# Optimization experiments

Hardware: AMD Instinct MI355X
Metric: run time of the kernel (lower is better)

## Reference

```python
import jax, jax.numpy as jnp
import numpy as np

B, L, D, H = 4, 1024, 1024, 16
DH = D // H  # 64
TOPK = 32


def setup_inputs() -> dict:
    key = jax.random.key(0)
    ks = jax.random.split(key, 9)
    s = 1.0 / np.sqrt(D)
    return {
        "x": jax.random.normal(ks[0], (B, L, D), jnp.float32),
        "Wq": jax.random.normal(ks[1], (D, D), jnp.float32) * s,
        "bq": jax.random.normal(ks[2], (D,), jnp.float32) * 0.01,
        "Wk": jax.random.normal(ks[3], (D, D), jnp.float32) * s,
        "bk": jax.random.normal(ks[4], (D,), jnp.float32) * 0.01,
        "Wv": jax.random.normal(ks[5], (D, D), jnp.float32) * s,
        "bv": jax.random.normal(ks[6], (D,), jnp.float32) * 0.01,
        "Wo": jax.random.normal(ks[7], (D, D), jnp.float32) * s,
        "bo": jax.random.normal(ks[8], (D,), jnp.float32) * 0.01,
        "top_k": TOPK,
    }


def reference(x, Wq, bq, Wk, bk, Wv, bv, Wo, bo, top_k):
    b, l, _ = x.shape
    q = (x @ Wq + bq).reshape(b, l, H, DH)
    k = (x @ Wk + bk).reshape(b, l, H, DH)
    v = (x @ Wv + bv).reshape(b, l, H, DH)
    # scores: [B, i, j, h]
    scores = jnp.einsum('bihd,bjhd->bijh', q, k) / np.sqrt(DH).astype(np.float32)
    # softmax over axis 2 (j), as in the original (dim=2 of bijh)
    weights = jax.nn.softmax(scores, axis=2)
    if top_k is not None:
        # top-k along j: move j to last axis -> [B, i, h, j]
        w_t = jnp.swapaxes(weights, 2, 3)
        _, idx = jax.lax.top_k(w_t, top_k)
        mask = jnp.put_along_axis(jnp.zeros_like(w_t), idx, 1.0, axis=-1, inplace=False)
        w_t = w_t * mask
        w_t = w_t / (jnp.sum(w_t, axis=-1, keepdims=True) + 1e-8)
        weights = jnp.swapaxes(w_t, 2, 3)
    attn = jnp.einsum('bijh,bjhd->bihd', weights, v).reshape(b, l, D)
    return attn @ Wo + bo
```

## Files before the change

### kernel.cpp

```cpp
#include <hip/hip_runtime.h>
#include <math.h>

#define B_ 4
#define L_ 1024
#define D_ 1024
#define H_ 16
#define DH_ 64
#define M_ (B_*L_)

typedef _Float16 half8 __attribute__((ext_vector_type(8)));
typedef _Float16 half4 __attribute__((ext_vector_type(4)));
typedef float f32x4 __attribute__((ext_vector_type(4)));

#define MFMA16(a,b,c) __builtin_amdgcn_mfma_f32_16x16x32_f16(a, b, c, 0, 0, 0)

__global__ __launch_bounds__(256) void split_x(const float* __restrict__ x,
                                               _Float16* __restrict__ xh,
                                               _Float16* __restrict__ xl) {
  const int i = blockIdx.x * 256 + threadIdx.x;
  float4 v = ((const float4*)x)[i];
  const float a0 = v.x * 16.f, a1 = v.y * 16.f, a2 = v.z * 16.f, a3 = v.w * 16.f;
  const _Float16 h0 = (_Float16)a0, h1 = (_Float16)a1, h2 = (_Float16)a2, h3 = (_Float16)a3;
  half4 hv, lv;
  hv[0] = h0; hv[1] = h1; hv[2] = h2; hv[3] = h3;
  lv[0] = (_Float16)(a0 - (float)h0);
  lv[1] = (_Float16)(a1 - (float)h1);
  lv[2] = (_Float16)(a2 - (float)h2);
  lv[3] = (_Float16)(a3 - (float)h3);
  ((half4*)xh)[i] = hv;
  ((half4*)xl)[i] = lv;
}

__global__ __launch_bounds__(256) void split_wt(const float* __restrict__ W,
                                                _Float16* __restrict__ Wh,
                                                _Float16* __restrict__ Wl) {
  __shared__ float tile[64][65];
  const int t = threadIdx.x;
  const int tk = blockIdx.x & 15;
  const int tn = blockIdx.x >> 4;
  const int kr = t >> 2, ns = (t & 3) * 16;
  const float* src = W + (size_t)(tk * 64 + kr) * D_ + tn * 64 + ns;
  float4 v0 = ((const float4*)src)[0];
  float4 v1 = ((const float4*)src)[1];
  float4 v2 = ((const float4*)src)[2];
  float4 v3 = ((const float4*)src)[3];
  tile[ns + 0][kr] = v0.x;  tile[ns + 1][kr] = v0.y;  tile[ns + 2][kr] = v0.z;  tile[ns + 3][kr] = v0.w;
  tile[ns + 4][kr] = v1.x;  tile[ns + 5][kr] = v1.y;  tile[ns + 6][kr] = v1.z;  tile[ns + 7][kr] = v1.w;
  tile[ns + 8][kr] = v2.x;  tile[ns + 9][kr] = v2.y;  tile[ns + 10][kr] = v2.z; tile[ns + 11][kr] = v2.w;
  tile[ns + 12][kr] = v3.x; tile[ns + 13][kr] = v3.y; tile[ns + 14][kr] = v3.z; tile[ns + 15][kr] = v3.w;
  __syncthreads();
  const int nr = t >> 2, ks = (t & 3) * 16;
  const float* tr = &tile[nr][ks];
  half8 hv0, hv1, lv0, lv1;
#pragma unroll
  for (int i = 0; i < 8; i++) {
    const float s0 = tr[i] * 512.f;
    const float s1 = tr[i + 8] * 512.f;
    const _Float16 h0 = (_Float16)s0, h1 = (_Float16)s1;
    hv0[i] = h0; hv1[i] = h1;
    lv0[i] = (_Float16)(s0 - (float)h0);
    lv1[i] = (_Float16)(s1 - (float)h1);
  }
  _Float16* dh = Wh + (size_t)(tn * 64 + nr) * D_ + tk * 64 + ks;
  _Float16* dl = Wl + (size_t)(tn * 64 + nr) * D_ + tk * 64 + ks;
  *(half8*)dh = hv0; *(half8*)(dh + 8) = hv1;
  *(half8*)dl = lv0; *(half8*)(dl + 8) = lv1;
}

__device__ __forceinline__ void gemm_f16x3_body(
    const _Float16* __restrict__ Ah, const _Float16* __restrict__ Al,
    const _Float16* __restrict__ Bh, const _Float16* __restrict__ Bl,
    const float* __restrict__ bias, float* __restrict__ Cf,
    _Float16* __restrict__ Ch, _Float16* __restrict__ Cl, const bool f16out) {
  __shared__ __align__(16) _Float16 sA[2][2][128][32];
  __shared__ __align__(16) _Float16 sB[2][2][128][32];
  const int t = threadIdx.x;
  const int lane = t & 63;
  const int wid = t >> 6;
  const int bm = blockIdx.y * 128;
  const int bn = blockIdx.x * 128;

  const int m0 = t >> 2, sp0 = t & 3;
  const int sl0 = sp0 ^ ((m0 >> 1) & 3);
  const int m1 = m0 + 64;
  const _Float16* gA0h = Ah + (size_t)(bm + m0) * D_ + sl0 * 8;
  const _Float16* gA1h = Ah + (size_t)(bm + m1) * D_ + sl0 * 8;
  const _Float16* gA0l = Al + (size_t)(bm + m0) * D_ + sl0 * 8;
  const _Float16* gA1l = Al + (size_t)(bm + m1) * D_ + sl0 * 8;
  const _Float16* gB0h = Bh + (size_t)(bn + m0) * D_ + sl0 * 8;
  const _Float16* gB1h = Bh + (size_t)(bn + m1) * D_ + sl0 * 8;
  const _Float16* gB0l = Bl + (size_t)(bn + m0) * D_ + sl0 * 8;
  const _Float16* gB1l = Bl + (size_t)(bn + m1) * D_ + sl0 * 8;

  half8 rA0h = *(const half8*)(gA0h);
  half8 rA1h = *(const half8*)(gA1h);
  half8 rA0l = *(const half8*)(gA0l);
  half8 rA1l = *(const half8*)(gA1l);
  half8 rB0h = *(const half8*)(gB0h);
  half8 rB1h = *(const half8*)(gB1h);
  half8 rB0l = *(const half8*)(gB0l);
  half8 rB1l = *(const half8*)(gB1l);
  *(half8*)&sA[0][0][m0][sp0 * 8] = rA0h;
  *(half8*)&sA[0][0][m1][sp0 * 8] = rA1h;
  *(half8*)&sA[0][1][m0][sp0 * 8] = rA0l;
  *(half8*)&sA[0][1][m1][sp0 * 8] = rA1l;
  *(half8*)&sB[0][0][m0][sp0 * 8] = rB0h;
  *(half8*)&sB[0][0][m1][sp0 * 8] = rB1h;
  *(half8*)&sB[0][1][m0][sp0 * 8] = rB0l;
  *(half8*)&sB[0][1][m1][sp0 * 8] = rB1l;
  __syncthreads();

  f32x4 acc[4][4];
#pragma unroll
  for (int i = 0; i < 4; i++)
#pragma unroll
    for (int j = 0; j < 4; j++) acc[i][j] = {0.f, 0.f, 0.f, 0.f};

  const int wr = wid >> 1, wc = wid & 1;
  const int l15 = lane & 15;
  const int soff = ((lane >> 4) ^ ((l15 >> 1) & 3)) * 8;

  int p = 0;
  for (int k0 = 0; k0 < 1024; k0 += 32) {
    const bool more = (k0 + 32) < 1024;
    if (more) {
      const int kk = k0 + 32;
      rA0h = *(const half8*)(gA0h + kk);
      rA1h = *(const half8*)(gA1h + kk);
      rA0l = *(const half8*)(gA0l + kk);
      rA1l = *(const half8*)(gA1l + kk);
      rB0h = *(const half8*)(gB0h + kk);
      rB1h = *(const half8*)(gB1h + kk);
      rB0l = *(const half8*)(gB0l + kk);
      rB1l = *(const half8*)(gB1l + kk);
    }
    half8 bh[4], bl[4];
#pragma unroll
    for (int ni = 0; ni < 4; ni++) {
      const int rb = wc * 64 + ni * 16 + l15;
      bh[ni] = *(const half8*)&sB[p][0][rb][soff];
      bl[ni] = *(const half8*)&sB[p][1][rb][soff];
    }
#pragma unroll
    for (int mi = 0; mi < 4; mi++) {
      const int ra = wr * 64 + mi * 16 + l15;
      const half8 ah = *(const half8*)&sA[p][0][ra][soff];
      const half8 al = *(const half8*)&sA[p][1][ra][soff];
#pragma unroll
      for (int ni = 0; ni < 4; ni++) {
        acc[mi][ni] = MFMA16(ah, bh[ni], acc[mi][ni]);
        acc[mi][ni] = MFMA16(ah, bl[ni], acc[mi][ni]);
        acc[mi][ni] = MFMA16(al, bh[ni], acc[mi][ni]);
      }
    }
    if (more) {
      const int q = p ^ 1;
      *(half8*)&sA[q][0][m0][sp0 * 8] = rA0h;
      *(half8*)&sA[q][0][m1][sp0 * 8] = rA1h;
      *(half8*)&sA[q][1][m0][sp0 * 8] = rA0l;
      *(half8*)&sA[q][1][m1][sp0 * 8] = rA1l;
      *(half8*)&sB[q][0][m0][sp0 * 8] = rB0h;
      *(half8*)&sB[q][0][m1][sp0 * 8] = rB1h;
      *(half8*)&sB[q][1][m0][sp0 * 8] = rB0l;
      *(half8*)&sB[q][1][m1][sp0 * 8] = rB1l;
      __syncthreads();
      p = q;
    }
  }

  const float inv = 1.0f / 8192.0f;
  const int orow = bm + wr * 64 + (lane >> 4) * 4;
  const int ocol = bn + wc * 64 + l15;
#pragma unroll
  for (int ni = 0; ni < 4; ni++) {
    const int col = ocol + ni * 16;
    const float bv = bias[col];
#pragma unroll
    for (int mi = 0; mi < 4; mi++) {
      const f32x4 a = acc[mi][ni];
#pragma unroll
      for (int r = 0; r < 4; r++) {
        const size_t idx = (size_t)(orow + mi * 16 + r) * D_ + col;
        const float val = a[r] * inv + bv;
        if (f16out) {
          const float vs = val * 16.0f;
          const _Float16 hh = (_Float16)vs;
          Ch[idx] = hh;
          Cl[idx] = (_Float16)(vs - (float)hh);
        } else {
          Cf[idx] = val;
        }
      }
    }
  }
}

__global__ __launch_bounds__(256, 2) void gemm_qkv_f16(
    const _Float16* __restrict__ xh, const _Float16* __restrict__ xl,
    const _Float16* __restrict__ Whq, const _Float16* __restrict__ Wlq,
    const _Float16* __restrict__ Whk, const _Float16* __restrict__ Wlk,
    const _Float16* __restrict__ Whv, const _Float16* __restrict__ Wlv,
    const float* __restrict__ bq, const float* __restrict__ bk, const float* __restrict__ bv,
    _Float16* __restrict__ qh, _Float16* __restrict__ ql,
    _Float16* __restrict__ kh, _Float16* __restrict__ kl,
    float* __restrict__ vf) {
  const int z = blockIdx.z;
  const _Float16* Bh = (z == 0) ? Whq : (z == 1) ? Whk : Whv;
  const _Float16* Bl = (z == 0) ? Wlq : (z == 1) ? Wlk : Wlv;
  const float* bias = (z == 0) ? bq : (z == 1) ? bk : bv;
  if (z == 2) {
    gemm_f16x3_body(xh, xl, Bh, Bl, bias, vf, nullptr, nullptr, false);
  } else {
    _Float16* Ch = (z == 0) ? qh : kh;
    _Float16* Cl = (z == 0) ? ql : kl;
    gemm_f16x3_body(xh, xl, Bh, Bl, bias, nullptr, Ch, Cl, true);
  }
}

__global__ __launch_bounds__(256, 2) void gemm_out_f16(
    const _Float16* __restrict__ ah, const _Float16* __restrict__ al,
    const _Float16* __restrict__ bh, const _Float16* __restrict__ bl,
    const float* __restrict__ bias, float* __restrict__ C) {
  gemm_f16x3_body(ah, al, bh, bl, bias, C, nullptr, nullptr, false);
}

#define SSWZ(row) (((row) & 7) << 2)

__global__ __launch_bounds__(512, 4) void attn_topk_mfma(
    const _Float16* __restrict__ qh, const _Float16* __restrict__ ql,
    const _Float16* __restrict__ kh, const _Float16* __restrict__ kl,
    const float* __restrict__ vf,
    _Float16* __restrict__ awh, _Float16* __restrict__ awl) {
  __shared__ float S[8][1024];
  __shared__ int   cidx[8][64];
  __shared__ float cfe[8][64];
  const int t = threadIdx.x;
  const int lane = t & 63;
  const int w = t >> 6;
  const int i0 = blockIdx.x * 8;
  const int h = blockIdx.y;
  const int b = blockIdx.z;
  const size_t rowbase = (size_t)b * L_;
  const int l15 = lane & 15;
  const int kgrp = lane >> 4;

  half8 Ahf[2], Alf[2];
#pragma unroll
  for (int ks = 0; ks < 2; ks++) {
    const size_t off = (rowbase + i0 + (l15 & 7)) * D_ + h * DH_ + ks * 32 + kgrp * 8;
    Ahf[ks] = *(const half8*)(qh + off);
    Alf[ks] = *(const half8*)(ql + off);
  }

  const float sscale = 1.0f / 2048.0f;
  for (int jt = 0; jt < 8; jt++) {
    const int j0 = w * 128 + jt * 16;
    const size_t koff = (rowbase + j0 + l15) * D_ + h * DH_ + kgrp * 8;
    const half8 Bh0 = *(const half8*)(kh + koff);
    const half8 Bh1 = *(const half8*)(kh + koff + 32);
    const half8 Bl0 = *(const half8*)(kl + koff);
    const half8 Bl1 = *(const half8*)(kl + koff + 32);
    f32x4 acc = {0.f, 0.f, 0.f, 0.f};
    acc = MFMA16(Ahf[0], Bh0, acc);
    acc = MFMA16(Ahf[1], Bh1, acc);
    acc = MFMA16(Ahf[0], Bl0, acc);
    acc = MFMA16(Ahf[1], Bl1, acc);
    acc = MFMA16(Alf[0], Bh0, acc);
    acc = MFMA16(Alf[1], Bh1, acc);
    if (kgrp < 2) {
      const int srow = kgrp * 4;
#pragma unroll
      for (int r = 0; r < 4; r++)
        S[srow + r][(j0 + l15) ^ SSWZ(srow + r)] = acc[r] * sscale;
    }
  }
  __syncthreads();

  const int row = w;
  const int swz = SSWZ(row);
  float sc[16];
#pragma unroll
  for (int u = 0; u < 16; u++) sc[u] = S[row][(u * 64 + lane) ^ swz];

  float mx = sc[0];
#pragma unroll
  for (int u = 1; u < 16; u++) mx = fmaxf(mx, sc[u]);
#pragma unroll
  for (int off = 32; off >= 1; off >>= 1) mx = fmaxf(mx, __shfl_xor(mx, off, 64));

  float lo = mx - 16.f, hi = mx;
  for (int it = 0; it < 14; ++it) {
    float mid = 0.5f * (lo + hi);
    int cnt = 0;
#pragma unroll
    for (int u = 0; u < 16; u++) cnt += __popcll(__ballot(sc[u] >= mid));
    if (cnt >= 32) lo = mid; else hi = mid;
  }
  int cabove = 0;
#pragma unroll
  for (int u = 0; u < 16; u++) cabove += __popcll(__ballot(sc[u] >= hi));
  float v31 = hi;
  while (cabove < 32) {
    float nx = -INFINITY;
#pragma unroll
    for (int u = 0; u < 16; u++) nx = fmaxf(nx, (sc[u] < v31) ? sc[u] : -INFINITY);
#pragma unroll
    for (int off = 32; off >= 1; off >>= 1) nx = fmaxf(nx, __shfl_xor(nx, off, 64));
    int ceq = 0;
#pragma unroll
    for (int u = 0; u < 16; u++) ceq += __popcll(__ballot(sc[u] == nx));
    cabove += ceq;
    v31 = nx;
  }
  int c_eq = 0;
#pragma unroll
  for (int u = 0; u < 16; u++) c_eq += __popcll(__ballot(sc[u] == v31));
  const int c_gt = cabove - c_eq;
  const bool span = (cabove > 32);
  const int keep_eq = 32 - c_gt;
  float v32;
  if (span) {
    v32 = v31;
  } else {
    float nx = -INFINITY;
#pragma unroll
    for (int u = 0; u < 16; u++) nx = fmaxf(nx, (sc[u] < v31) ? sc[u] : -INFINITY);
#pragma unroll
    for (int off = 32; off >= 1; off >>= 1) nx = fmaxf(nx, __shfl_xor(nx, off, 64));
    v32 = nx;
  }
  const float tau = 0.5f * (v31 + v32);
  const float invbeta = 166666.67f;

  float z = 0.f;
#pragma unroll
  for (int u = 0; u < 16; u++) z += __expf(sc[u] - mx);
#pragma unroll
  for (int off = 32; off >= 1; off >>= 1) z += __shfl_xor(z, off, 64);

  bool band = false;
  if (!span) {
    int inband = 0;
#pragma unroll
    for (int u = 0; u < 16; u++)
      inband |= (fabsf(sc[u] - tau) <= 1.81e-4f) ? 1 : 0;
    band = (__ballot(inband) != 0ull);
  }

  const float cutoff = fminf(tau - 1.8e-4f, v31);
  const float* vcol = vf + rowbase * D_ + h * DH_ + lane;
  float o;
  bool fast = false;
  if (!span) {
    int run = 0;
    float psum = 0.f;
#pragma unroll
    for (int u = 0; u < 16; u++) {
      unsigned long long m = __ballot(sc[u] >= cutoff);
      if (sc[u] >= cutoff) {
        const float eu = __expf(sc[u] - mx);
        float feu;
        if (band) {
          float arg = (sc[u] - tau) * invbeta;
          float fwv = (arg > 30.f) ? 1.f : ((arg < -30.f) ? 0.f : 1.f / (1.f + __expf(-arg)));
          feu = fwv * eu;
        } else {
          feu = (sc[u] > tau) ? eu : 0.f;
        }
        int pos = run + (int)__popcll(m & ((1ull << lane) - 1ull));
        if (pos < 64) { cidx[w][pos] = u * 64 + lane; cfe[w][pos] = feu; }
        psum += feu;
      }
      run += (int)__popcll(m);
    }
    if (run <= 64) {
      fast = true;
      float Ssum = psum;
#pragma unroll
      for (int off = 32; off >= 1; off >>= 1) Ssum += __shfl_xor(Ssum, off, 64);
      const int npad = (run + 7) & ~7;
      if (lane < npad - run) { cidx[w][run + lane] = 0; cfe[w][run + lane] = 0.f; }
      float acc = 0.f;
      for (int c = 0; c < npad; c += 8) {
        int jx[8]; float fx[8]; float vv[8];
#pragma unroll
        for (int i = 0; i < 8; i++) { jx[i] = cidx[w][c + i]; fx[i] = cfe[w][c + i]; }
#pragma unroll
        for (int i = 0; i < 8; i++) vv[i] = vcol[(size_t)jx[i] * D_];
#pragma unroll
        for (int i = 0; i < 8; i++) acc = fmaf(fx[i], vv[i], acc);
      }
      o = acc / (Ssum + 1e-8f * z);
    }
  }
  if (!fast) {
    float Ssum = 0.f, acc = 0.f;
    int eq_seen = 0;
    for (int u = 0; u < 16; ++u) {
      unsigned long long mask = __ballot(sc[u] >= cutoff);
      while (mask) {
        int l2 = (int)__builtin_ctzll(mask);
        mask &= mask - 1;
        float s_ = __shfl(sc[u], l2, 64);
        float e_ = __expf(s_ - mx);
        float f_;
        if (span) {
          if (s_ > v31) f_ = 1.f;
          else if (s_ == v31) { f_ = (eq_seen < keep_eq) ? 1.f : 0.f; ++eq_seen; }
          else f_ = 0.f;
        } else {
          float arg = (s_ - tau) * invbeta;
          f_ = (arg > 30.f) ? 1.f : ((arg < -30.f) ? 0.f : 1.f / (1.f + __expf(-arg)));
        }
        float fe_ = f_ * e_;
        Ssum += fe_;
        acc = fmaf(fe_, vcol[(size_t)(u * 64 + l2) * D_], acc);
      }
    }
    o = acc / (Ssum + 1e-8f * z);
  }

  const float os = o * 16.0f;
  const _Float16 oh = (_Float16)os;
  const size_t oidx = (rowbase + i0 + row) * D_ + h * DH_ + lane;
  awh[oidx] = oh;
  awl[oidx] = (_Float16)(os - (float)oh);
}

extern "C" void kernel_launch(void* const* d_in, const int* in_sizes, int n_in,
                              void* d_out, int out_size, void* d_ws, size_t ws_size,
                              hipStream_t stream) {
  const float* x  = (const float*)d_in[0];
  const float* Wq = (const float*)d_in[1];
  const float* bq = (const float*)d_in[2];
  const float* Wk = (const float*)d_in[3];
  const float* bk = (const float*)d_in[4];
  const float* Wv = (const float*)d_in[5];
  const float* bv = (const float*)d_in[6];
  const float* Wo = (const float*)d_in[7];
  const float* bo = (const float*)d_in[8];
  float* out = (float*)d_out;

  const size_t MD = (size_t)M_ * D_;
  const size_t WD = (size_t)D_ * D_;
  float* slot0 = (float*)d_ws;
  float* slot1 = slot0 + MD;
  float* vf    = slot1 + MD;
  float* slot3 = vf + MD;
  float* slot4 = slot3 + MD;

  _Float16* qh = (_Float16*)slot0;  _Float16* ql = qh + MD;
  _Float16* kh = (_Float16*)slot1;  _Float16* kl = kh + MD;
  _Float16* xh = (_Float16*)slot3;  _Float16* xl = xh + MD;
  _Float16* awh = xh;
  _Float16* awl = xl;
  _Float16* Whq = (_Float16*)slot4;
  _Float16* Wlq = Whq + WD;
  _Float16* Whk = Wlq + WD;
  _Float16* Wlk = Whk + WD;
  _Float16* Whv = Wlk + WD;
  _Float16* Wlv = Whv + WD;
  _Float16* Who = Wlv + WD;
  _Float16* Wlo = Who + WD;

  dim3 b256(256);
  hipLaunchKernelGGL(split_x, dim3(4096), b256, 0, stream, x, xh, xl);
  hipLaunchKernelGGL(split_wt, dim3(256), b256, 0, stream, Wq, Whq, Wlq);
  hipLaunchKernelGGL(split_wt, dim3(256), b256, 0, stream, Wk, Whk, Wlk);
  hipLaunchKernelGGL(split_wt, dim3(256), b256, 0, stream, Wv, Whv, Wlv);
  hipLaunchKernelGGL(split_wt, dim3(256), b256, 0, stream, Wo, Who, Wlo);
  hipLaunchKernelGGL(gemm_qkv_f16, dim3(8, 32, 3), b256, 0, stream,
                     xh, xl, Whq, Wlq, Whk, Wlk, Whv, Wlv, bq, bk, bv,
                     qh, ql, kh, kl, vf);
  hipLaunchKernelGGL(attn_topk_mfma, dim3(128, 16, 4), dim3(512), 0, stream,
                     qh, ql, kh, kl, vf, awh, awl);
  hipLaunchKernelGGL(gemm_out_f16, dim3(8, 32), b256, 0, stream,
                     awh, awl, Who, Wlo, bo, out);
}
```

Before: 500.6 us.

## Halve attention block to 4 waves, two rows per wave, DPP reductions

The attention top-k kernel now runs 256 threads per block, so each wave computes scores for 256 keys and then handles two query rows, interleaving the bisection and selection work for both rows. Wavefront max and sum reductions switch from shfl_xor loops to DPP row operations plus a readlane. The aim is more independent work per wave to hide ballot and reduction latency, and cheaper cross-lane reductions. The cost is doubled per-wave register state, which may reduce occupancy under the new launch bounds.

Measured after the change: 523.6 us. 1.05x slower.

```diff
diff --git a/kernel.cpp b/kernel.cpp
--- a/kernel.cpp
+++ b/kernel.cpp
@@ -13,6 +13,28 @@
 typedef float f32x4 __attribute__((ext_vector_type(4)));
 
 #define MFMA16(a,b,c) __builtin_amdgcn_mfma_f32_16x16x32_f16(a, b, c, 0, 0, 0)
+
+#define DPPF(oldv, x, ctrl, rmask) \
+  __int_as_float(__builtin_amdgcn_update_dpp(__float_as_int(oldv), __float_as_int(x), ctrl, rmask, 0xf, false))
+
+__device__ __forceinline__ float wfred_max(float x) {
+  x = fmaxf(x, DPPF(-INFINITY, x, 0x111, 0xf));
+  x = fmaxf(x, DPPF(-INFINITY, x, 0x112, 0xf));
+  x = fmaxf(x, DPPF(-INFINITY, x, 0x114, 0xf));
+  x = fmaxf(x, DPPF(-INFINITY, x, 0x118, 0xf));
+  x = fmaxf(x, DPPF(-INFINITY, x, 0x142, 0xa));
+  x = fmaxf(x, DPPF(-INFINITY, x, 0x143, 0xc));
+  return __int_as_float(__builtin_amdgcn_readlane(__float_as_int(x), 63));
+}
+__device__ __forceinline__ float wfred_sum(float x) {
+  x = x + DPPF(0.f, x, 0x111, 0xf);
+  x = x + DPPF(0.f, x, 0x112, 0xf);
+  x = x + DPPF(0.f, x, 0x114, 0xf);
+  x = x + DPPF(0.f, x, 0x118, 0xf);
+  x = x + DPPF(0.f, x, 0x142, 0xa);
+  x = x + DPPF(0.f, x, 0x143, 0xc);
+  return __int_as_float(__builtin_amdgcn_readlane(__float_as_int(x), 63));
+}
 
 __global__ __launch_bounds__(256) void split_x(const float* __restrict__ x,
                                                _Float16* __restrict__ xh,
@@ -226,7 +248,7 @@
 
 #define SSWZ(row) (((row) & 7) << 2)
 
-__global__ __launch_bounds__(512, 4) void attn_topk_mfma(
+__global__ __launch_bounds__(256, 4) void attn_topk_mfma(
     const _Float16* __restrict__ qh, const _Float16* __restrict__ ql,
     const _Float16* __restrict__ kh, const _Float16* __restrict__ kl,
     const float* __restrict__ vf,
@@ -253,8 +275,8 @@
   }
 
   const float sscale = 1.0f / 2048.0f;
-  for (int jt = 0; jt < 8; jt++) {
-    const int j0 = w * 128 + jt * 16;
+  for (int jt = 0; jt < 16; jt++) {
+    const int j0 = w * 256 + jt * 16;
     const size_t koff = (rowbase + j0 + l15) * D_ + h * DH_ + kgrp * 8;
     const half8 Bh0 = *(const half8*)(kh + koff);
     const half8 Bh1 = *(const half8*)(kh + koff + 32);
@@ -276,155 +298,182 @@
   }
   __syncthreads();
 
-  const int row = w;
-  const int swz = SSWZ(row);
-  float sc[16];
-#pragma unroll
-  for (int u = 0; u < 16; u++) sc[u] = S[row][(u * 64 + lane) ^ swz];
-
-  float mx = sc[0];
-#pragma unroll
-  for (int u = 1; u < 16; u++) mx = fmaxf(mx, sc[u]);
-#pragma unroll
-  for (int off = 32; off >= 1; off >>= 1) mx = fmaxf(mx, __shfl_xor(mx, off, 64));
-
-  float lo = mx - 16.f, hi = mx;
+  float sc[2][16];
+#pragma unroll
+  for (int rr = 0; rr < 2; rr++) {
+    const int row = w * 2 + rr;
+    const int swz = SSWZ(row);
+#pragma unroll
+    for (int u = 0; u < 16; u++) sc[rr][u] = S[row][(u * 64 + lane) ^ swz];
+  }
+
+  float mx[2];
+#pragma unroll
+  for (int rr = 0; rr < 2; rr++) {
+    float m = sc[rr][0];
+#pragma unroll
+    for (int u = 1; u < 16; u++) m = fmaxf(m, sc[rr][u]);
+    mx[rr] = wfred_max(m);
+  }
+
+  float lo[2], hi[2];
+#pragma unroll
+  for (int rr = 0; rr < 2; rr++) { lo[rr] = mx[rr] - 16.f; hi[rr] = mx[rr]; }
   for (int it = 0; it < 14; ++it) {
-    float mid = 0.5f * (lo + hi);
-    int cnt = 0;
-#pragma unroll
-    for (int u = 0; u < 16; u++) cnt += __popcll(__ballot(sc[u] >= mid));
-    if (cnt >= 32) lo = mid; else hi = mid;
-  }
-  int cabove = 0;
-#pragma unroll
-  for (int u = 0; u < 16; u++) cabove += __popcll(__ballot(sc[u] >= hi));
-  float v31 = hi;
-  while (cabove < 32) {
-    float nx = -INFINITY;
-#pragma unroll
-    for (int u = 0; u < 16; u++) nx = fmaxf(nx, (sc[u] < v31) ? sc[u] : -INFINITY);
-#pragma unroll
-    for (int off = 32; off >= 1; off >>= 1) nx = fmaxf(nx, __shfl_xor(nx, off, 64));
-    int ceq = 0;
-#pragma unroll
-    for (int u = 0; u < 16; u++) ceq += __popcll(__ballot(sc[u] == nx));
-    cabove += ceq;
-    v31 = nx;
-  }
-  int c_eq = 0;
-#pragma unroll
-  for (int u = 0; u < 16; u++) c_eq += __popcll(__ballot(sc[u] == v31));
-  const int c_gt = cabove - c_eq;
-  const bool span = (cabove > 32);
-  const int keep_eq = 32 - c_gt;
-  float v32;
-  if (span) {
-    v32 = v31;
-  } else {
-    float nx = -INFINITY;
-#pragma unroll
-    for (int u = 0; u < 16; u++) nx = fmaxf(nx, (sc[u] < v31) ? sc[u] : -INFINITY);
-#pragma unroll
-    for (int off = 32; off >= 1; off >>= 1) nx = fmaxf(nx, __shfl_xor(nx, off, 64));
-    v32 = nx;
-  }
-  const float tau = 0.5f * (v31 + v32);
+#pragma unroll
+    for (int rr = 0; rr < 2; rr++) {
+      float mid = 0.5f * (lo[rr] + hi[rr]);
+      int cnt = 0;
+#pragma unroll
+      for (int u = 0; u < 16; u++) cnt += __popcll(__ballot(sc[rr][u] >= mid));
+      if (cnt >= 32) lo[rr] = mid; else hi[rr] = mid;
+    }
+  }
+
+  float v31a[2], v32a[2], tau[2];
+  bool span[2];
+  int keep_eq[2];
+#pragma unroll
+  for (int rr = 0; rr < 2; rr++) {
+    int cabove = 0;
+#pragma unroll
+    for (int u = 0; u < 16; u++) cabove += __popcll(__ballot(sc[rr][u] >= hi[rr]));
+    float v31 = hi[rr];
+    while (cabove < 32) {
+      float nx = -INFINITY;
+#pragma unroll
+      for (int u = 0; u < 16; u++) nx = fmaxf(nx, (sc[rr][u] < v31) ? sc[rr][u] : -INFINITY);
+      nx = wfred_max(nx);
+      int ceq = 0;
+#pragma unroll
+      for (int u = 0; u < 16; u++) ceq += __popcll(__ballot(sc[rr][u] == nx));
+      cabove += ceq;
+      v31 = nx;
+    }
+    int c_eq = 0;
+#pragma unroll
+    for (int u = 0; u < 16; u++) c_eq += __popcll(__ballot(sc[rr][u] == v31));
+    const int c_gt = cabove - c_eq;
+    span[rr] = (cabove > 32);
+    keep_eq[rr] = 32 - c_gt;
+    float v32;
+    if (span[rr]) {
+      v32 = v31;
+    } else {
+      float nx = -INFINITY;
+#pragma unroll
+      for (int u = 0; u < 16; u++) nx = fmaxf(nx, (sc[rr][u] < v31) ? sc[rr][u] : -INFINITY);
+      nx = wfred_max(nx);
+      v32 = nx;
+    }
+    v31a[rr] = v31; v32a[rr] = v32;
+    tau[rr] = 0.5f * (v31 + v32);
+  }
   const float invbeta = 166666.67f;
 
-  float z = 0.f;
-#pragma unroll
-  for (int u = 0; u < 16; u++) z += __expf(sc[u] - mx);
-#pragma unroll
-  for (int off = 32; off >= 1; off >>= 1) z += __shfl_xor(z, off, 64);
-
-  bool band = false;
-  if (!span) {
-    int inband = 0;
-#pragma unroll
-    for (int u = 0; u < 16; u++)
-      inband |= (fabsf(sc[u] - tau) <= 1.81e-4f) ? 1 : 0;
-    band = (__ballot(inband) != 0ull);
-  }
-
-  const float cutoff = fminf(tau - 1.8e-4f, v31);
+  float zz[2];
+#pragma unroll
+  for (int rr = 0; rr < 2; rr++) {
+    float zl = 0.f;
+#pragma unroll
+    for (int u = 0; u < 16; u++) zl += __expf(sc[rr][u] - mx[rr]);
+    zz[rr] = wfred_sum(zl);
+  }
+
+  bool band[2];
+#pragma unroll
+  for (int rr = 0; rr < 2; rr++) {
+    band[rr] = false;
+    if (!span[rr]) {
+      int inband = 0;
+#pragma unroll
+      for (int u = 0; u < 16; u++)
+        inband |= (fabsf(sc[rr][u] - tau[rr]) <= 1.81e-4f) ? 1 : 0;
+      band[rr] = (__ballot(inband) != 0ull);
+    }
+  }
+
   const float* vcol = vf + rowbase * D_ + h * DH_ + lane;
-  float o;
-  bool fast = false;
-  if (!span) {
-    int run = 0;
-    float psum = 0.f;
-#pragma unroll
-    for (int u = 0; u < 16; u++) {
-      unsigned long long m = __ballot(sc[u] >= cutoff);
-      if (sc[u] >= cutoff) {
-        const float eu = __expf(sc[u] - mx);
-        float feu;
-        if (band) {
-          float arg = (sc[u] - tau) * invbeta;
-          float fwv = (arg > 30.f) ? 1.f : ((arg < -30.f) ? 0.f : 1.f / (1.f + __expf(-arg)));
-          feu = fwv * eu;
-        } else {
-          feu = (sc[u] > tau) ? eu : 0.f;
+
+#pragma unroll
+  for (int rr = 0; rr < 2; rr++) {
+    const int row = w * 2 + rr;
+    const float cutoff = fminf(tau[rr] - 1.8e-4f, v31a[rr]);
+    float o;
+    bool fast = false;
+    if (!span[rr]) {
+      int run = 0;
+      float psum = 0.f;
+#pragma unroll
+      for (int u = 0; u < 16; u++) {
+        unsigned long long m = __ballot(sc[rr][u] >= cutoff);
+        if (sc[rr][u] >= cutoff) {
+          const float eu = __expf(sc[rr][u] - mx[rr]);
+          float feu;
+          if (band[rr]) {
+            float arg = (sc[rr][u] - tau[rr]) * invbeta;
+            float fwv = (arg > 30.f) ? 1.f : ((arg < -30.f) ? 0.f : 1.f / (1.f + __expf(-arg)));
+            feu = fwv * eu;
+          } else {
+            feu = (sc[rr][u] > tau[rr]) ? eu : 0.f;
+          }
+          int pos = run + (int)__popcll(m & ((1ull << lane) - 1ull));
+          if (pos < 64) { cidx[row][pos] = u * 64 + lane; cfe[row][pos] = feu; }
+          psum += feu;
         }
-        int pos = run + (int)__popcll(m & ((1ull << lane) - 1ull));
-        if (pos < 64) { cidx[w][pos] = u * 64 + lane; cfe[w][pos] = feu; }
-        psum += feu;
+        run += (int)__popcll(m);
       }
-      run += (int)__popcll(m);
-    }
-    if (run <= 64) {
-      fast = true;
-      float Ssum = psum;
-#pragma unroll
-      for (int off = 32; off >= 1; off >>= 1) Ssum += __shfl_xor(Ssum, off, 64);
-      const int npad = (run + 7) & ~7;
-      if (lane < npad - run) { cidx[w][run + lane] = 0; cfe[w][run + lane] = 0.f; }
-      float acc = 0.f;
-      for (int c = 0; c < npad; c += 8) {
-        int jx[8]; float fx[8]; float vv[8];
-#pragma unroll
-        for (int i = 0; i < 8; i++) { jx[i] = cidx[w][c + i]; fx[i] = cfe[w][c + i]; }
-#pragma unroll
-        for (int i = 0; i < 8; i++) vv[i] = vcol[(size_t)jx[i] * D_];
-#pragma unroll
-        for (int i = 0; i < 8; i++) acc = fmaf(fx[i], vv[i], acc);
+      if (run <= 64) {
+        fast = true;
+        const float Ssum = wfred_sum(psum);
+        const int npad = (run + 7) & ~7;
+        if (lane < npad - run) { cidx[row][run + lane] = 0; cfe[row][run + lane] = 0.f; }
+        float acc = 0.f;
+        for (int c = 0; c < npad; c += 8) {
+          int jx[8]; float fx[8]; float vv[8];
+#pragma unroll
+          for (int i = 0; i < 8; i++) { jx[i] = cidx[row][c + i]; fx[i] = cfe[row][c + i]; }
+#pragma unroll
+          for (int i = 0; i < 8; i++) vv[i] = vcol[(size_t)jx[i] * D_];
+#pragma unroll
+          for (int i = 0; i < 8; i++) acc = fmaf(fx[i], vv[i], acc);
+        }
+        o = acc / (Ssum + 1e-8f * zz[rr]);
       }
-      o = acc / (Ssum + 1e-8f * z);
-    }
-  }
-  if (!fast) {
-    float Ssum = 0.f, acc = 0.f;
-    int eq_seen = 0;
-    for (int u = 0; u < 16; ++u) {
-      unsigned long long mask = __ballot(sc[u] >= cutoff);
-      while (mask) {
-        int l2 = (int)__builtin_ctzll(mask);
-        mask &= mask - 1;
-        float s_ = __shfl(sc[u], l2, 64);
-        float e_ = __expf(s_ - mx);
-        float f_;
-        if (span) {
-          if (s_ > v31) f_ = 1.f;
-          else if (s_ == v31) { f_ = (eq_seen < keep_eq) ? 1.f : 0.f; ++eq_seen; }
-          else f_ = 0.f;
-        } else {
-          float arg = (s_ - tau) * invbeta;
-          f_ = (arg > 30.f) ? 1.f : ((arg < -30.f) ? 0.f : 1.f / (1.f + __expf(-arg)));
+    }
+    if (!fast) {
+      float Ssum = 0.f, acc = 0.f;
+      int eq_seen = 0;
+      for (int u = 0; u < 16; ++u) {
+        unsigned long long mask = __ballot(sc[rr][u] >= cutoff);
+        while (mask) {
+          int l2 = (int)__builtin_ctzll(mask);
+          mask &= mask - 1;
+          float s_ = __shfl(sc[rr][u], l2, 64);
+          float e_ = __expf(s_ - mx[rr]);
+          float f_;
+          if (span[rr]) {
+            if (s_ > v31a[rr]) f_ = 1.f;
+            else if (s_ == v31a[rr]) { f_ = (eq_seen < keep_eq[rr]) ? 1.f : 0.f; ++eq_seen; }
+            else f_ = 0.f;
+          } else {
+            float arg = (s_ - tau[rr]) * invbeta;
+            f_ = (arg > 30.f) ? 1.f : ((arg < -30.f) ? 0.f : 1.f / (1.f + __expf(-arg)));
+          }
+          float fe_ = f_ * e_;
+          Ssum += fe_;
+          acc = fmaf(fe_, vcol[(size_t)(u * 64 + l2) * D_], acc);
         }
-        float fe_ = f_ * e_;
-        Ssum += fe_;
-        acc = fmaf(fe_, vcol[(size_t)(u * 64 + l2) * D_], acc);
       }
-    }
-    o = acc / (Ssum + 1e-8f * z);
-  }
-
-  const float os = o * 16.0f;
-  const _Float16 oh = (_Float16)os;
-  const size_t oidx = (rowbase + i0 + row) * D_ + h * DH_ + lane;
-  awh[oidx] = oh;
-  awl[oidx] = (_Float16)(os - (float)oh);
+      o = acc / (Ssum + 1e-8f * zz[rr]);
+    }
+
+    const float os = o * 16.0f;
+    const _Float16 oh = (_Float16)os;
+    const size_t oidx = (rowbase + i0 + row) * D_ + h * DH_ + lane;
+    awh[oidx] = oh;
+    awl[oidx] = (_Float16)(os - (float)oh);
+  }
 }
 
 extern "C" void kernel_launch(void* const* d_in, const int* in_sizes, int n_in,
@@ -472,7 +521,7 @@
   hipLaunchKernelGGL(gemm_qkv_f16, dim3(8, 32, 3), b256, 0, stream,
                      xh, xl, Whq, Wlq, Whk, Wlk, Whv, Wlv, bq, bk, bv,
                      qh, ql, kh, kl, vf);
-  hipLaunchKernelGGL(attn_topk_mfma, dim3(128, 16, 4), dim3(512), 0, stream,
+  hipLaunchKernelGGL(attn_topk_mfma, dim3(128, 16, 4), b256, 0, stream,
                      qh, ql, kh, kl, vf, awh, awl);
   hipLaunchKernelGGL(gemm_out_f16, dim3(8, 32), b256, 0, stream,
                      awh, awl, Who, Wlo, bo, out);
```
